# Kernel tuning notes

Hardware: AMD Instinct MI355X
Metric: run time of the kernel (lower is better)

## Reference

```python
import jax, jax.numpy as jnp
import numpy as np

D_MODEL = 512
TEMP = 30.0  # softmax temperature used by TransformerTrack-style RelationUnit
EPS = 1e-5
NORM_SCALE = float(np.sqrt(1.0 / (D_MODEL * 4 * 4)))


def _instance_l2norm(x):
    # x: [n, hw, b, d]; InstanceL2Norm over (dim, h, w) per (image, batch) sample
    n, hw, b, d = x.shape
    ss = jnp.sum(x * x, axis=(1, 3), keepdims=True)  # [n,1,b,1]
    return x * (NORM_SCALE * jnp.sqrt((d * hw) / (ss + EPS)))


def _cnorm(r, i):
    # joint L2 normalization of a complex vector along last axis
    s = jnp.sqrt(jnp.sum(r * r + i * i, axis=-1, keepdims=True) + 1e-12)
    return r / s, i / s


def _rel_self_attn(xr, xi, er, ei, WK):
    # xr/xi: [n, L, b, d]; er/ei: [n, L, L, b, dk] relative (helix) embeddings
    qr, qi = _cnorm(xr @ WK, xi @ WK)           # [n,L,b,dk]
    # real part of complex conjugate inner product <q, k>
    scores = (jnp.einsum('nqbk,nlbk->nbql', qr, qr)
              + jnp.einsum('nqbk,nlbk->nbql', qi, qi)
              + jnp.einsum('nqbk,nqlbk->nbql', qr, er)
              + jnp.einsum('nqbk,nqlbk->nbql', qi, ei))
    A = jax.nn.softmax(scores * TEMP, axis=-1)  # [n,b,q,l]
    out_r = jnp.einsum('nbql,nlbd->nqbd', A, xr)
    out_i = jnp.einsum('nbql,nlbd->nqbd', A, xi)
    return out_r, out_i


def _cross_attn(qr_in, qi_in, kr_in, ki_in, vr, vi, WK):
    # q: [Lq,b,d]; k,v: [Lk,b,d]
    qr, qi = _cnorm(qr_in @ WK, qi_in @ WK)
    kr, ki = _cnorm(kr_in @ WK, ki_in @ WK)
    scores = jnp.einsum('qbk,lbk->bql', qr, kr) + jnp.einsum('qbk,lbk->bql', qi, ki)
    A = jax.nn.softmax(scores * TEMP, axis=-1)
    out_r = jnp.einsum('bql,lbd->qbd', A, vr)
    out_i = jnp.einsum('bql,lbd->qbd', A, vi)
    return out_r, out_i


def _forward(src_real, src_imag, tgt_real, tgt_imag,
             src_emb_real, src_emb_imag, tgt_emb_real, tgt_emb_imag,
             pos_real, pos_imag, WK_rel, WK_cross):
    n, b, d, h, w = src_real.shape
    hw = h * w

    def tok(x):  # [n,b,d,h,w] -> [n,hw,b,d]
        return x.reshape(n, b, d, hw).transpose(0, 3, 1, 2)

    def emb(x):  # [n,b,dk,hw,hw] -> [n,hw,hw,b,dk]
        return x.transpose(0, 3, 4, 1, 2)

    sr, si = tok(src_real), tok(src_imag)
    tr, ti = tok(tgt_real), tok(tgt_imag)
    esr, esi = emb(src_emb_real), emb(src_emb_imag)
    etr, eti = emb(tgt_emb_real), emb(tgt_emb_imag)

    # ---- encoder (num_layers = 1) ----
    s2r, s2i = _rel_self_attn(sr, si, esr, esi, WK_rel)
    mem_r = _instance_l2norm(sr + s2r).reshape(n * hw, b, d)
    mem_i = _instance_l2norm(si + s2i).reshape(n * hw, b, d)

    # pos: [n,b,h,w] -> [n*hw, b, d] (broadcast over dim as in .repeat(1,1,dim))
    pr = jnp.broadcast_to(pos_real.reshape(n, b, hw).transpose(0, 2, 1).reshape(n * hw, b, 1), (n * hw, b, d))
    pi = jnp.broadcast_to(pos_imag.reshape(n, b, hw).transpose(0, 2, 1).reshape(n * hw, b, 1), (n * hw, b, d))

    def IN3(x):
        return _instance_l2norm(x.reshape(n, hw, b, d)).reshape(n * hw, b, d)

    # ---- decoder (num_layers = 1) ----
    t2r, t2i = _rel_self_attn(tr, ti, etr, eti, WK_rel)
    xr = _instance_l2norm(tr + t2r).reshape(n * hw, b, d)
    xi = _instance_l2norm(ti + t2i).reshape(n * hw, b, d)

    mask_r, mask_i = _cross_attn(xr, xi, mem_r, mem_i, pr, pi, WK_cross)
    y2r = IN3(xr * mask_r)
    y2i = IN3(xi * mask_i)

    t3r, t3i = _cross_attn(xr, xi, mem_r, mem_i, mem_r * pr, mem_i * pi, WK_cross)
    y4r = IN3(xr + t3r)
    y4i = IN3(xi + t3i)

    out_r = IN3(y2r + y4r)
    out_i = IN3(y2i + y4i)

    feat_r = out_r.reshape(n, h, w, b, d).transpose(0, 3, 4, 1, 2).reshape(n * b, d, h, w)
    feat_i = out_i.reshape(n, h, w, b, d).transpose(0, 3, 4, 1, 2).reshape(n * b, d, h, w)
    return out_r, out_i, feat_r, feat_i


def setup_inputs() -> dict:
    key = jax.random.key(0)
    ks = jax.random.split(key, 12)
    n, b, d, h, dk = 2, 2, 512, 16, 64
    hw = h * h
    inp = {
        'src_real': jax.random.normal(ks[0], (n, b, d, h, h), jnp.float32),
        'src_imag': jax.random.normal(ks[1], (n, b, d, h, h), jnp.float32),
        'tgt_real': jax.random.normal(ks[2], (n, b, d, h, h), jnp.float32),
        'tgt_imag': jax.random.normal(ks[3], (n, b, d, h, h), jnp.float32),
        'src_emb_real': jax.random.normal(ks[4], (n, b, dk, hw, hw), jnp.float32),
        'src_emb_imag': jax.random.normal(ks[5], (n, b, dk, hw, hw), jnp.float32),
        'tgt_emb_real': jax.random.normal(ks[6], (n, b, dk, hw, hw), jnp.float32),
        'tgt_emb_imag': jax.random.normal(ks[7], (n, b, dk, hw, hw), jnp.float32),
        'pos_real': jax.random.uniform(ks[8], (n, b, h, h), jnp.float32),
        'pos_imag': jax.random.uniform(ks[9], (n, b, h, h), jnp.float32),
        'WK_rel': jax.random.normal(ks[10], (d, dk), jnp.float32) * 0.02,
        'WK_cross': jax.random.normal(ks[11], (d, 128), jnp.float32) * 0.02,
    }
    return inp


def reference(src_real, src_imag, tgt_real, tgt_imag,
              src_emb_real, src_emb_imag, tgt_emb_real, tgt_emb_imag,
              pos_real, pos_imag, WK_rel, WK_cross):
    return _forward(src_real, src_imag, tgt_real, tgt_imag,
                    src_emb_real, src_emb_imag, tgt_emb_real, tgt_emb_imag,
                    pos_real, pos_imag, WK_rel, WK_cross)
```

## Files before the change

### kernel.cpp

```cpp
#include <hip/hip_runtime.h>
#include <cstdint>
#include <cstddef>

#define N_ 2
#define B_ 2
#define D_ 512
#define HW_ 256
#define DK_ 64
#define DKC_ 128
#define G_ 4
#define NBLK_ 32

constexpr size_t OFF_TSR = 0;
constexpr size_t OFF_TSI = 524288;
constexpr size_t OFF_TTR = 1048576;
constexpr size_t OFF_TTI = 1572864;
constexpr size_t OFF_QSR = 2097152;
constexpr size_t OFF_QSI = OFF_QSR + 65536;
constexpr size_t OFF_QTR = OFF_QSI + 65536;
constexpr size_t OFF_QTI = OFF_QTR + 65536;
constexpr size_t OFF_AS  = OFF_QTI + 65536;
constexpr size_t OFF_AT  = OFF_AS + 262144;
constexpr size_t OFF_YSR = OFF_AT + 262144;
constexpr size_t OFF_YSI = OFF_YSR + 524288;
constexpr size_t OFF_YTR = OFF_YSI + 524288;
constexpr size_t OFF_YTI = OFF_YTR + 524288;
constexpr size_t OFF_QCR = OFF_YTI + 524288;
constexpr size_t OFF_QCI = OFF_QCR + 131072;
constexpr size_t OFF_KCR = OFF_QCI + 131072;
constexpr size_t OFF_KCI = OFF_KCR + 131072;
constexpr size_t OFF_AC  = OFF_KCI + 131072;
constexpr size_t OFF_T3R = OFF_AC + 524288;
constexpr size_t OFF_T3I = OFF_T3R + 524288;
constexpr size_t OFF_MR  = OFF_T3I + 524288;
constexpr size_t OFF_MI  = OFF_MR + 1024;
constexpr size_t OFF_P1  = OFF_MI + 1024;
constexpr size_t OFF_P2  = OFF_P1 + 512;
constexpr size_t OFF_P3  = OFF_P2 + 512;
constexpr size_t OFF_S1  = OFF_P3 + 256;
constexpr size_t OFF_S2  = OFF_S1 + 16;
constexpr size_t OFF_SZ  = OFF_S2 + 16;

template<int NT>
__device__ __forceinline__ float blk_sum(float v, float* sh) {
  int tid = threadIdx.x;
  sh[tid] = v; __syncthreads();
  #pragma unroll
  for (int s = NT/2; s > 0; s >>= 1) { if (tid < s) sh[tid] += sh[tid+s]; __syncthreads(); }
  float r = sh[0]; __syncthreads(); return r;
}
template<int NT>
__device__ __forceinline__ float blk_max(float v, float* sh) {
  int tid = threadIdx.x;
  sh[tid] = v; __syncthreads();
  #pragma unroll
  for (int s = NT/2; s > 0; s >>= 1) { if (tid < s) sh[tid] = fmaxf(sh[tid], sh[tid+s]); __syncthreads(); }
  float r = sh[0]; __syncthreads(); return r;
}

__global__ void k_transpose(const float* sR, const float* sI, const float* tR, const float* tI, float* ws) {
  int which = blockIdx.y;
  const float* in = (which==0)? sR : (which==1)? sI : (which==2)? tR : tI;
  float* out = ws + ((which==0)? OFF_TSR : (which==1)? OFF_TSI : (which==2)? OFF_TTR : OFF_TTI);
  int bx = blockIdx.x;
  int pt = bx & 3, dt = (bx>>2)&7, nb = bx>>5;
  int ni = nb>>1, bi = nb&1;
  __shared__ float tile[64][65];
  int tid = threadIdx.x;
  int p0 = pt*64, d0 = dt*64;
  #pragma unroll
  for (int it=0; it<16; ++it) {
    int i = it*256 + tid; int row = i>>6, col = i&63;
    tile[row][col] = in[(size_t)(nb*D_ + d0+row)*HW_ + p0+col];
  }
  __syncthreads();
  #pragma unroll
  for (int it=0; it<16; ++it) {
    int i = it*256 + tid; int row = i>>6, col = i&63;
    out[(size_t)((ni*HW_ + p0+row)*B_ + bi)*D_ + d0+col] = tile[col][row];
  }
}

__global__ void k_qrel(float* ws, const float* WK) {
  int idx = blockIdx.x;
  int which = idx >> 10; int t = idx & 1023;
  int r = t >> 1, bi = t & 1;
  const float* Tr = ws + (which ? OFF_TTR : OFF_TSR);
  const float* Ti = ws + (which ? OFF_TTI : OFF_TSI);
  float* Qr = ws + (which ? OFF_QTR : OFF_QSR);
  float* Qi = ws + (which ? OFF_QTI : OFF_QSI);
  int tid = threadIdx.x;
  int kk = tid & 63, isIm = tid >> 6;
  const float* x = (isIm ? Ti : Tr) + (size_t)(r*B_ + bi)*D_;
  const float4* x4 = (const float4*)x;
  float acc = 0.f;
  #pragma unroll 8
  for (int d4 = 0; d4 < 128; ++d4) {
    float4 xv = x4[d4]; int d = d4*4;
    acc += xv.x*WK[(d+0)*DK_+kk] + xv.y*WK[(d+1)*DK_+kk] + xv.z*WK[(d+2)*DK_+kk] + xv.w*WK[(d+3)*DK_+kk];
  }
  __shared__ float sh[128];
  float ss = blk_sum<128>(acc*acc, sh);
  float q = acc / sqrtf(ss + 1e-12f);
  (isIm ? Qi : Qr)[(size_t)(r*B_ + bi)*DK_ + kk] = q;
}

__global__ void __launch_bounds__(128) k_gram(float* ws) {
  int bx = blockIdx.x;
  int lt = bx & 3, qt = (bx>>2)&7, nb = (bx>>5)&3, which = bx>>7;
  int ni = nb>>1, bi = nb&1;
  const float* Qr = ws + (which ? OFF_QTR : OFF_QSR);
  const float* Qi = ws + (which ? OFF_QTI : OFF_QSI);
  float* A = ws + (which ? OFF_AT : OFF_AS) + (size_t)nb*65536;
  __shared__ float Qrs[32][33], Qis[32][33], Krs[32][68], Kis[32][68];
  int tid = threadIdx.x, ty = tid>>4, tx = tid&15;
  int ty4 = ty*4, tx4 = tx*4;
  float acc[4][4] = {};
  for (int c = 0; c < 2; ++c) {
    #pragma unroll
    for (int it = 0; it < 8; ++it) {
      int i = it*128 + tid; int row = i>>5, col = i&31;
      size_t qa = (size_t)((ni*HW_ + qt*32+row)*B_ + bi)*DK_ + c*32 + col;
      Qrs[row][col] = Qr[qa];
      Qis[row][col] = Qi[qa];
    }
    #pragma unroll
    for (int it = 0; it < 16; ++it) {
      int i = it*128 + tid; int kk = i&31, col = i>>5;
      size_t ka = (size_t)((ni*HW_ + lt*64+col)*B_ + bi)*DK_ + c*32 + kk;
      Krs[kk][col] = Qr[ka];
      Kis[kk][col] = Qi[ka];
    }
    __syncthreads();
    #pragma unroll
    for (int kk = 0; kk < 32; ++kk) {
      float4 kr = *(const float4*)&Krs[kk][tx4];
      float4 ki = *(const float4*)&Kis[kk][tx4];
      #pragma unroll
      for (int i = 0; i < 4; ++i) {
        float qr = Qrs[ty4+i][kk], qi = Qis[ty4+i][kk];
        acc[i][0] += qr*kr.x + qi*ki.x;
        acc[i][1] += qr*kr.y + qi*ki.y;
        acc[i][2] += qr*kr.z + qi*ki.z;
        acc[i][3] += qr*kr.w + qi*ki.w;
      }
    }
    __syncthreads();
  }
  #pragma unroll
  for (int i = 0; i < 4; ++i)
    #pragma unroll
    for (int j = 0; j < 4; ++j)
      A[(size_t)(qt*32+ty4+i)*256 + lt*64+tx4+j] = acc[i][j];
}

__global__ void __launch_bounds__(256) k_selfattn(float* ws, const float* esr, const float* esi,
                                                  const float* etr, const float* eti) {
  int idx = blockIdx.x;
  int iq = idx & 255, nb = (idx>>8)&3, which = idx>>10;
  int ni = nb>>1, bi = nb&1;
  const float* Qr = ws + (which ? OFF_QTR : OFF_QSR);
  const float* Qi = ws + (which ? OFF_QTI : OFF_QSI);
  const float* er = which ? etr : esr;
  const float* ei = which ? eti : esi;
  float* Arow = ws + (which ? OFF_AT : OFF_AS) + (size_t)nb*65536 + (size_t)iq*256;
  int tid = threadIdx.x, w = tid>>6, lane = tid&63;
  size_t qbase = (size_t)((ni*HW_ + iq)*B_ + bi)*DK_ + w*16;
  int kl = lane & 15;
  float qv = ((lane & 16) ? Qi : Qr)[qbase + kl];
  int l0 = lane*4;
  float a0=0.f, a1=0.f, a2=0.f, a3=0.f;
  size_t eb = (size_t)nb*4194304 + (size_t)(w*16)*65536 + (size_t)iq*256 + l0;
  #pragma unroll 4
  for (int kk = 0; kk < 16; ++kk) {
    float4 e4r = *(const float4*)&er[eb + (size_t)kk*65536];
    float4 e4i = *(const float4*)&ei[eb + (size_t)kk*65536];
    float fr = __shfl(qv, kk);
    float fi = __shfl(qv, 16+kk);
    a0 += fr*e4r.x + fi*e4i.x;
    a1 += fr*e4r.y + fi*e4i.y;
    a2 += fr*e4r.z + fi*e4i.z;
    a3 += fr*e4r.w + fi*e4i.w;
  }
  __shared__ float part[4][256];
  __shared__ float sh[256];
  *(float4*)&part[w][l0] = make_float4(a0,a1,a2,a3);
  __syncthreads();
  float s = (part[0][tid]+part[1][tid]+part[2][tid]+part[3][tid] + Arow[tid]) * 30.f;
  float m = blk_max<256>(s, sh);
  float e = __expf(s - m);
  float sum = blk_sum<256>(e, sh);
  Arow[tid] = e / sum;
}

__global__ void __launch_bounds__(128) k_selfapply(float* ws) {
  int bx = blockIdx.x;
  int dt = bx & 7, qt = (bx>>3)&7, nb = (bx>>6)&3, which = bx>>8;
  int ni = nb>>1, bi = nb&1;
  const float* A  = ws + (which ? OFF_AT : OFF_AS) + (size_t)nb*65536;
  const float* Xr = ws + (which ? OFF_TTR : OFF_TSR);
  const float* Xi = ws + (which ? OFF_TTI : OFF_TSI);
  float* Yr = ws + (which ? OFF_YTR : OFF_YSR);
  float* Yi = ws + (which ? OFF_YTI : OFF_YSI);
  __shared__ float As[32][33], Xrs[32][68], Xis[32][68];
  int tid = threadIdx.x, ty = tid>>4, tx = tid&15;
  int ty4 = ty*4, tx4 = tx*4;
  float ar[4][4] = {}, ai[4][4] = {};
  for (int c = 0; c < 8; ++c) {
    #pragma unroll
    for (int it = 0; it < 8; ++it) {
      int i = it*128 + tid; int row = i>>5, col = i&31;
      As[row][col] = A[(size_t)(qt*32+row)*256 + c*32+col];
    }
    #pragma unroll
    for (int it = 0; it < 16; ++it) {
      int i = it*128 + tid; int row = i>>6, col = i&63;
      size_t xb = (size_t)((ni*HW_ + c*32+row)*B_ + bi)*D_ + dt*64+col;
      Xrs[row][col] = Xr[xb]; Xis[row][col] = Xi[xb];
    }
    __syncthreads();
    #pragma unroll
    for (int kk = 0; kk < 32; ++kk) {
      float4 vr = *(const float4*)&Xrs[kk][tx4];
      float4 vi = *(const float4*)&Xis[kk][tx4];
      #pragma unroll
      for (int i = 0; i < 4; ++i) {
        float a = As[ty4+i][kk];
        ar[i][0] += a*vr.x; ar[i][1] += a*vr.y; ar[i][2] += a*vr.z; ar[i][3] += a*vr.w;
        ai[i][0] += a*vi.x; ai[i][1] += a*vi.y; ai[i][2] += a*vi.z; ai[i][3] += a*vi.w;
      }
    }
    __syncthreads();
  }
  #pragma unroll
  for (int i = 0; i < 4; ++i) {
    size_t o = (size_t)((ni*HW_ + qt*32 + ty4+i)*B_ + bi)*D_ + dt*64 + tx4;
    #pragma unroll
    for (int j = 0; j < 4; ++j) { Yr[o+j] = Xr[o+j] + ar[i][j]; Yi[o+j] = Xi[o+j] + ai[i][j]; }
  }
}

__global__ void k_reduce4(float* ws) {
  int qy = blockIdx.y;
  const float* a = ws + ((qy==0)? OFF_YSR : (qy==1)? OFF_YSI : (qy==2)? OFF_YTR : OFF_YTI);
  int g = blockIdx.x / NBLK_, blk = blockIdx.x % NBLK_;
  int ni = g>>1, bi = g&1;
  int tid = threadIdx.x;
  float acc = 0.f;
  for (int p = blk; p < HW_; p += NBLK_) {
    const float* row = a + (size_t)((ni*HW_ + p)*B_ + bi)*D_;
    for (int d = tid; d < D_; d += 256) { float v = row[d]; acc += v*v; }
  }
  __shared__ float sh[256];
  float s = blk_sum<256>(acc, sh);
  if (!tid) ws[OFF_P1 + (size_t)(qy*G_ + g)*NBLK_ + blk] = s;
}

__global__ void k_finalize(const float* part, float* scales, int nq) {
  int t = threadIdx.x;
  if (t < nq) {
    float ss = 0.f;
    for (int j = 0; j < NBLK_; ++j) ss += part[t*NBLK_ + j];
    scales[t] = 4.f * rsqrtf(ss + 1e-5f);
  }
}

__global__ void k_applyscale(float* ws, const float* scales) {
  int qy = blockIdx.y;
  float* a = ws + ((qy==0)? OFF_YSR : (qy==1)? OFF_YSI : (qy==2)? OFF_YTR : OFF_YTI);
  int idx4 = blockIdx.x*256 + threadIdx.x;
  int elem = idx4*4;
  int bi = (elem / D_) & 1;
  int r = elem >> 10;
  int ni = r >> 8;
  float s = scales[qy*G_ + ni*2 + bi];
  float4 v = ((float4*)a)[idx4];
  v.x *= s; v.y *= s; v.z *= s; v.w *= s;
  ((float4*)a)[idx4] = v;
}

__global__ void k_crossproj(float* ws, const float* W) {
  int idx = blockIdx.x;
  int isK = idx >> 10; int t = idx & 1023;
  int r = t >> 1, bi = t & 1;
  const float* inR = ws + (isK ? OFF_YSR : OFF_YTR);
  const float* inI = ws + (isK ? OFF_YSI : OFF_YTI);
  float* oR = ws + (isK ? OFF_KCR : OFF_QCR);
  float* oI = ws + (isK ? OFF_KCI : OFF_QCI);
  int tid = threadIdx.x;
  const float4* xr4 = (const float4*)(inR + (size_t)(r*B_ + bi)*D_);
  const float4* xi4 = (const float4*)(inI + (size_t)(r*B_ + bi)*D_);
  float aR = 0.f, aI = 0.f;
  #pragma unroll 8
  for (int d4 = 0; d4 < 128; ++d4) {
    float4 rv = xr4[d4], iv = xi4[d4]; int d = d4*4;
    float w0 = W[(d+0)*DKC_ + tid], w1 = W[(d+1)*DKC_ + tid], w2 = W[(d+2)*DKC_ + tid], w3 = W[(d+3)*DKC_ + tid];
    aR += rv.x*w0 + rv.y*w1 + rv.z*w2 + rv.w*w3;
    aI += iv.x*w0 + iv.y*w1 + iv.z*w2 + iv.w*w3;
  }
  __shared__ float sh[128];
  float ss = blk_sum<128>(aR*aR + aI*aI, sh);
  float inv = 1.f / sqrtf(ss + 1e-12f);
  oR[(size_t)(r*B_ + bi)*DKC_ + tid] = aR * inv;
  oI[(size_t)(r*B_ + bi)*DKC_ + tid] = aI * inv;
}

__global__ void __launch_bounds__(128) k_crossscore(float* ws) {
  int bx = blockIdx.x;
  int lt = bx & 7, qt = (bx>>3)&15, bi = bx>>7;
  const float* Qr = ws + OFF_QCR; const float* Qi = ws + OFF_QCI;
  const float* Kr = ws + OFF_KCR; const float* Ki = ws + OFF_KCI;
  float* S = ws + OFF_AC + (size_t)bi*262144;
  __shared__ float Qrs[32][33], Qis[32][33], Krs[32][68], Kis[32][68];
  int tid = threadIdx.x, ty = tid>>4, tx = tid&15;
  int ty4 = ty*4, tx4 = tx*4;
  float acc[4][4] = {};
  for (int c = 0; c < 4; ++c) {
    #pragma unroll
    for (int it = 0; it < 8; ++it) {
      int i = it*128 + tid; int row = i>>5, col = i&31;
      Qrs[row][col] = Qr[(size_t)((qt*32+row)*B_ + bi)*DKC_ + c*32 + col];
      Qis[row][col] = Qi[(size_t)((qt*32+row)*B_ + bi)*DKC_ + c*32 + col];
    }
    #pragma unroll
    for (int it = 0; it < 16; ++it) {
      int i = it*128 + tid; int kk = i&31, col = i>>5;
      Krs[kk][col] = Kr[(size_t)((lt*64+col)*B_ + bi)*DKC_ + c*32 + kk];
      Kis[kk][col] = Ki[(size_t)((lt*64+col)*B_ + bi)*DKC_ + c*32 + kk];
    }
    __syncthreads();
    #pragma unroll
    for (int kk = 0; kk < 32; ++kk) {
      float4 kr = *(const float4*)&Krs[kk][tx4];
      float4 ki = *(const float4*)&Kis[kk][tx4];
      #pragma unroll
      for (int i = 0; i < 4; ++i) {
        float qr = Qrs[ty4+i][kk], qi = Qis[ty4+i][kk];
        acc[i][0] += qr*kr.x + qi*ki.x;
        acc[i][1] += qr*kr.y + qi*ki.y;
        acc[i][2] += qr*kr.z + qi*ki.z;
        acc[i][3] += qr*kr.w + qi*ki.w;
      }
    }
    __syncthreads();
  }
  #pragma unroll
  for (int i = 0; i < 4; ++i)
    #pragma unroll
    for (int j = 0; j < 4; ++j)
      S[(size_t)(qt*32+ty4+i)*512 + lt*64+tx4+j] = acc[i][j];
}

__global__ void k_softmaxrow(float* ws, const float* posr, const float* posi) {
  int bx = blockIdx.x;
  int bi = bx >> 9, iq = bx & 511;
  float* row = ws + OFF_AC + (size_t)bi*262144 + (size_t)iq*512;
  int tid = threadIdx.x;
  float s0 = row[tid]*30.f, s1 = row[tid+256]*30.f;
  __shared__ float sh[256];
  float m = blk_max<256>(fmaxf(s0, s1), sh);
  float e0 = __expf(s0 - m), e1 = __expf(s1 - m);
  float sum = blk_sum<256>(e0 + e1, sh);
  float inv = 1.f / sum;
  float a0 = e0*inv, a1 = e1*inv;
  row[tid] = a0; row[tid+256] = a1;
  float pr0 = posr[bi*HW_ + tid],        pr1 = posr[(B_+bi)*HW_ + tid];
  float pi0 = posi[bi*HW_ + tid],        pi1 = posi[(B_+bi)*HW_ + tid];
  float mr = blk_sum<256>(a0*pr0 + a1*pr1, sh);
  float mi = blk_sum<256>(a0*pi0 + a1*pi1, sh);
  if (!tid) { ws[OFF_MR + bi*512 + iq] = mr; ws[OFF_MI + bi*512 + iq] = mi; }
}

__global__ void __launch_bounds__(128) k_crossapply(float* ws, const float* posr, const float* posi) {
  int bx = blockIdx.x;
  int dt = bx & 7, qt = (bx>>3)&15, bi = (bx>>7)&1, kc = bx>>8;
  const float* A  = ws + OFF_AC + (size_t)bi*262144;
  const float* Mr = ws + OFF_YSR; const float* Mi = ws + OFF_YSI;
  float* Pr = ws + (kc ? OFF_TSR : OFF_T3R);
  float* Pi = ws + (kc ? OFF_TSI : OFF_T3I);
  __shared__ float As[32][33], Vrs[32][68], Vis[32][68];
  int tid = threadIdx.x, ty = tid>>4, tx = tid&15;
  int ty4 = ty*4, tx4 = tx*4;
  float ar[4][4] = {}, ai[4][4] = {};
  for (int c = 0; c < 8; ++c) {
    int kb = kc*256 + c*32;
    #pragma unroll
    for (int it = 0; it < 8; ++it) {
      int i = it*128 + tid; int row = i>>5, col = i&31;
      As[row][col] = A[(size_t)(qt*32+row)*512 + kb+col];
    }
    #pragma unroll
    for (int it = 0; it < 16; ++it) {
      int i = it*128 + tid; int row = i>>6, col = i&63;
      int l = kb + row; int nil = l>>8, pl = l&255;
      float pvr = posr[(nil*B_ + bi)*HW_ + pl];
      float pvi = posi[(nil*B_ + bi)*HW_ + pl];
      size_t vb = (size_t)(l*B_ + bi)*D_ + dt*64+col;
      Vrs[row][col] = Mr[vb] * pvr;
      Vis[row][col] = Mi[vb] * pvi;
    }
    __syncthreads();
    #pragma unroll
    for (int kk = 0; kk < 32; ++kk) {
      float4 vr = *(const float4*)&Vrs[kk][tx4];
      float4 vi = *(const float4*)&Vis[kk][tx4];
      #pragma unroll
      for (int i = 0; i < 4; ++i) {
        float a = As[ty4+i][kk];
        ar[i][0] += a*vr.x; ar[i][1] += a*vr.y; ar[i][2] += a*vr.z; ar[i][3] += a*vr.w;
        ai[i][0] += a*vi.x; ai[i][1] += a*vi.y; ai[i][2] += a*vi.z; ai[i][3] += a*vi.w;
      }
    }
    __syncthreads();
  }
  #pragma unroll
  for (int i = 0; i < 4; ++i) {
    size_t o = (size_t)((qt*32+ty4+i)*B_ + bi)*D_ + dt*64 + tx4;
    #pragma unroll
    for (int j = 0; j < 4; ++j) { Pr[o+j] = ar[i][j]; Pi[o+j] = ai[i][j]; }
  }
}

__global__ void k_reducey24(float* ws) {
  int qy = blockIdx.y;
  int g = blockIdx.x / NBLK_, blk = blockIdx.x % NBLK_;
  int ni = g>>1, bi = g&1;
  const float* X   = ws + ((qy==0 || qy==2) ? OFF_YTR : OFF_YTI);
  const float* T3a = ws + ((qy==2) ? OFF_T3R : OFF_T3I);
  const float* T3b = ws + ((qy==2) ? OFF_TSR : OFF_TSI);
  const float* M   = ws + ((qy==0) ? OFF_MR : OFF_MI);
  int tid = threadIdx.x;
  float acc = 0.f;
  for (int p = blk; p < HW_; p += NBLK_) {
    int l = ni*HW_ + p;
    size_t rb = (size_t)(l*B_ + bi)*D_;
    if (qy < 2) {
      float m = M[bi*512 + l];
      for (int d = tid; d < D_; d += 256) { float v = X[rb+d]*m; acc += v*v; }
    } else {
      for (int d = tid; d < D_; d += 256) { float v = X[rb+d] + T3a[rb+d] + T3b[rb+d]; acc += v*v; }
    }
  }
  __shared__ float sh[256];
  float s = blk_sum<256>(acc, sh);
  if (!tid) ws[OFF_P2 + (size_t)(qy*G_ + g)*NBLK_ + blk] = s;
}

__global__ void k_combine(float* ws, const float* scales2) {
  int y = blockIdx.y;
  int g = blockIdx.x / NBLK_, blk = blockIdx.x % NBLK_;
  int ni = g>>1, bi = g&1;
  const float* X   = ws + (y ? OFF_YTI : OFF_YTR);
  float* T3a       = ws + (y ? OFF_T3I : OFF_T3R);
  const float* T3b = ws + (y ? OFF_TSI : OFF_TSR);
  const float* M   = ws + (y ? OFF_MI : OFF_MR);
  float a2 = scales2[y*G_ + g], a4 = scales2[(2+y)*G_ + g];
  int tid = threadIdx.x;
  float acc = 0.f;
  for (int p = blk; p < HW_; p += NBLK_) {
    int l = ni*HW_ + p;
    float m = M[bi*512 + l];
    size_t rb = (size_t)(l*B_ + bi)*D_;
    for (int d = tid; d < D_; d += 256) {
      float x = X[rb+d];
      float z = a2*(x*m) + a4*(x + T3a[rb+d] + T3b[rb+d]);
      T3a[rb+d] = z;
      acc += z*z;
    }
  }
  __shared__ float sh[256];
  float s = blk_sum<256>(acc, sh);
  if (!tid) ws[OFF_P3 + (size_t)(y*G_ + g)*NBLK_ + blk] = s;
}

__global__ void k_final(float* ws, const float* scalesZ, float* out) {
  int y = blockIdx.y;
  int bx = blockIdx.x;
  int pt = bx & 3, dt = (bx>>2)&7, nb = bx>>5;
  int ni = nb>>1, bi = nb&1;
  const float* Z = ws + (y ? OFF_T3I : OFF_T3R);
  float s = scalesZ[y*G_ + nb];
  float* o1 = out + (size_t)y*524288;
  float* o2 = out + (size_t)(2+y)*524288;
  __shared__ float tile[64][65];
  int tid = threadIdx.x;
  int p0 = pt*64, d0 = dt*64;
  #pragma unroll
  for (int it = 0; it < 16; ++it) {
    int i = it*256 + tid; int row = i>>6, col = i&63;
    size_t idx = (size_t)((ni*HW_ + p0+row)*B_ + bi)*D_ + d0+col;
    float v = Z[idx] * s;
    o1[idx] = v;
    tile[row][col] = v;
  }
  __syncthreads();
  #pragma unroll
  for (int it = 0; it < 16; ++it) {
    int i = it*256 + tid; int row = i>>6, col = i&63;
    o2[(size_t)(nb*D_ + d0+row)*HW_ + p0+col] = tile[col][row];
  }
}

extern "C" void kernel_launch(void* const* d_in, const int* in_sizes, int n_in,
                              void* d_out, int out_size, void* d_ws, size_t ws_size,
                              hipStream_t stream) {
  const float* srcR = (const float*)d_in[0];
  const float* srcI = (const float*)d_in[1];
  const float* tgtR = (const float*)d_in[2];
  const float* tgtI = (const float*)d_in[3];
  const float* esr  = (const float*)d_in[4];
  const float* esi  = (const float*)d_in[5];
  const float* etr  = (const float*)d_in[6];
  const float* eti  = (const float*)d_in[7];
  const float* posR = (const float*)d_in[8];
  const float* posI = (const float*)d_in[9];
  const float* WKrel   = (const float*)d_in[10];
  const float* WKcross = (const float*)d_in[11];
  float* ws  = (float*)d_ws;
  float* out = (float*)d_out;

  k_transpose <<<dim3(128,4), 256, 0, stream>>>(srcR, srcI, tgtR, tgtI, ws);
  k_qrel      <<<2048, 128, 0, stream>>>(ws, WKrel);
  k_gram      <<<256, 128, 0, stream>>>(ws);
  k_selfattn  <<<2048, 256, 0, stream>>>(ws, esr, esi, etr, eti);
  k_selfapply <<<512, 128, 0, stream>>>(ws);
  k_reduce4   <<<dim3(G_*NBLK_,4), 256, 0, stream>>>(ws);
  k_finalize  <<<1, 64, 0, stream>>>(ws + OFF_P1, ws + OFF_S1, 16);
  k_applyscale<<<dim3(512,4), 256, 0, stream>>>(ws, ws + OFF_S1);
  k_crossproj <<<2048, 128, 0, stream>>>(ws, WKcross);
  k_crossscore<<<256, 128, 0, stream>>>(ws);
  k_softmaxrow<<<1024, 256, 0, stream>>>(ws, posR, posI);
  k_crossapply<<<512, 128, 0, stream>>>(ws, posR, posI);
  k_reducey24 <<<dim3(G_*NBLK_,4), 256, 0, stream>>>(ws);
  k_finalize  <<<1, 64, 0, stream>>>(ws + OFF_P2, ws + OFF_S2, 16);
  k_combine   <<<dim3(G_*NBLK_,2), 256, 0, stream>>>(ws, ws + OFF_S2);
  k_finalize  <<<1, 64, 0, stream>>>(ws + OFF_P3, ws + OFF_SZ, 8);
  k_final     <<<dim3(128,2), 256, 0, stream>>>(ws, ws + OFF_SZ, out);
}
```

Measured before the change: 275.0 us.

## Tile projection kernels over 8 rows and batch embedding loads in selfattn

The q-projection and cross-projection kernels now stage 8 token rows of real and imaginary input in shared memory and have each thread compute 2 or 4 output columns for both parts. Each weight row read is reused across real and imaginary parts, the block-wide reduction becomes a 32-lane shuffle reduction, and the block count drops eightfold. The self-attention kernel loads q into shared memory and issues all 16 embedding float4 loads per component up front to expose memory-level parallelism. The cost is higher register pressure, which the launch bound of 256 threads with 2 blocks tries to keep in check.

Measured after the change: 290.2 us. +5.6%, slower.

```diff
diff --git a/kernel.cpp b/kernel.cpp
--- a/kernel.cpp
+++ b/kernel.cpp
@@ -57,6 +57,11 @@
   for (int s = NT/2; s > 0; s >>= 1) { if (tid < s) sh[tid] = fmaxf(sh[tid], sh[tid+s]); __syncthreads(); }
   float r = sh[0]; __syncthreads(); return r;
 }
+__device__ __forceinline__ float wave_sum32(float v) {
+  #pragma unroll
+  for (int o = 16; o; o >>= 1) v += __shfl_xor(v, o, 64);
+  return v;
+}
 
 __global__ void k_transpose(const float* sR, const float* sI, const float* tR, const float* tI, float* ws) {
   int which = blockIdx.y;
@@ -81,28 +86,39 @@
   }
 }
 
-__global__ void k_qrel(float* ws, const float* WK) {
-  int idx = blockIdx.x;
-  int which = idx >> 10; int t = idx & 1023;
-  int r = t >> 1, bi = t & 1;
+__global__ void __launch_bounds__(256) k_qrel(float* ws, const float* WK) {
+  int bx = blockIdx.x;
+  int rg = bx & 127, which = bx >> 7;
   const float* Tr = ws + (which ? OFF_TTR : OFF_TSR);
   const float* Ti = ws + (which ? OFF_TTI : OFF_TSI);
   float* Qr = ws + (which ? OFF_QTR : OFF_QSR);
   float* Qi = ws + (which ? OFF_QTI : OFF_QSI);
-  int tid = threadIdx.x;
-  int kk = tid & 63, isIm = tid >> 6;
-  const float* x = (isIm ? Ti : Tr) + (size_t)(r*B_ + bi)*D_;
-  const float4* x4 = (const float4*)x;
-  float acc = 0.f;
-  #pragma unroll 8
-  for (int d4 = 0; d4 < 128; ++d4) {
-    float4 xv = x4[d4]; int d = d4*4;
-    acc += xv.x*WK[(d+0)*DK_+kk] + xv.y*WK[(d+1)*DK_+kk] + xv.z*WK[(d+2)*DK_+kk] + xv.w*WK[(d+3)*DK_+kk];
-  }
-  __shared__ float sh[128];
-  float ss = blk_sum<128>(acc*acc, sh);
-  float q = acc / sqrtf(ss + 1e-12f);
-  (isIm ? Qi : Qr)[(size_t)(r*B_ + bi)*DK_ + kk] = q;
+  int R0 = rg*8;
+  __shared__ float Xr[8][512], Xi[8][512];
+  int tid = threadIdx.x;
+  const float4* tr4 = (const float4*)(Tr + (size_t)R0*D_);
+  const float4* ti4 = (const float4*)(Ti + (size_t)R0*D_);
+  #pragma unroll
+  for (int it=0; it<4; ++it) {
+    int i = it*256 + tid;
+    ((float4*)&Xr[0][0])[i] = tr4[i];
+    ((float4*)&Xi[0][0])[i] = ti4[i];
+  }
+  __syncthreads();
+  int row = tid >> 5, col2 = (tid & 31)*2;
+  float a0r=0.f, a0i=0.f, a1r=0.f, a1i=0.f;
+  #pragma unroll 4
+  for (int d=0; d<512; ++d) {
+    float2 w = *(const float2*)&WK[(size_t)d*DK_ + col2];
+    float xr = Xr[row][d], xi = Xi[row][d];
+    a0r += xr*w.x; a1r += xr*w.y;
+    a0i += xi*w.x; a1i += xi*w.y;
+  }
+  float ss = wave_sum32(a0r*a0r + a1r*a1r + a0i*a0i + a1i*a1i);
+  float inv = 1.f / sqrtf(ss + 1e-12f);
+  size_t o = (size_t)(R0+row)*DK_ + col2;
+  Qr[o]   = a0r*inv; Qr[o+1] = a1r*inv;
+  Qi[o]   = a0i*inv; Qi[o+1] = a1i*inv;
 }
 
 __global__ void __launch_bounds__(128) k_gram(float* ws) {
@@ -154,8 +170,8 @@
       A[(size_t)(qt*32+ty4+i)*256 + lt*64+tx4+j] = acc[i][j];
 }
 
-__global__ void __launch_bounds__(256) k_selfattn(float* ws, const float* esr, const float* esi,
-                                                  const float* etr, const float* eti) {
+__global__ void __launch_bounds__(256, 2) k_selfattn(float* ws, const float* esr, const float* esi,
+                                                     const float* etr, const float* eti) {
   int idx = blockIdx.x;
   int iq = idx & 255, nb = (idx>>8)&3, which = idx>>10;
   int ni = nb>>1, bi = nb&1;
@@ -164,23 +180,31 @@
   const float* er = which ? etr : esr;
   const float* ei = which ? eti : esi;
   float* Arow = ws + (which ? OFF_AT : OFF_AS) + (size_t)nb*65536 + (size_t)iq*256;
+  __shared__ float qqr[64], qqi[64];
   int tid = threadIdx.x, w = tid>>6, lane = tid&63;
-  size_t qbase = (size_t)((ni*HW_ + iq)*B_ + bi)*DK_ + w*16;
-  int kl = lane & 15;
-  float qv = ((lane & 16) ? Qi : Qr)[qbase + kl];
+  int tokq = ni*HW_ + iq;
+  if (tid < 64)       qqr[tid]    = Qr[(size_t)(tokq*B_ + bi)*DK_ + tid];
+  else if (tid < 128) qqi[tid-64] = Qi[(size_t)(tokq*B_ + bi)*DK_ + (tid-64)];
+  __syncthreads();
+  float fr[16], fi[16];
+  #pragma unroll
+  for (int kk = 0; kk < 16; ++kk) { fr[kk] = qqr[w*16+kk]; fi[kk] = qqi[w*16+kk]; }
   int l0 = lane*4;
+  size_t eb = (size_t)nb*4194304 + (size_t)(w*16)*65536 + (size_t)iq*256 + l0;
+  const float4* er4 = (const float4*)&er[eb];
+  const float4* ei4 = (const float4*)&ei[eb];
+  float4 R[16], I[16];
+  #pragma unroll
+  for (int t = 0; t < 16; ++t) R[t] = er4[(size_t)t*16384];
+  #pragma unroll
+  for (int t = 0; t < 16; ++t) I[t] = ei4[(size_t)t*16384];
   float a0=0.f, a1=0.f, a2=0.f, a3=0.f;
-  size_t eb = (size_t)nb*4194304 + (size_t)(w*16)*65536 + (size_t)iq*256 + l0;
-  #pragma unroll 4
-  for (int kk = 0; kk < 16; ++kk) {
-    float4 e4r = *(const float4*)&er[eb + (size_t)kk*65536];
-    float4 e4i = *(const float4*)&ei[eb + (size_t)kk*65536];
-    float fr = __shfl(qv, kk);
-    float fi = __shfl(qv, 16+kk);
-    a0 += fr*e4r.x + fi*e4i.x;
-    a1 += fr*e4r.y + fi*e4i.y;
-    a2 += fr*e4r.z + fi*e4i.z;
-    a3 += fr*e4r.w + fi*e4i.w;
+  #pragma unroll
+  for (int t = 0; t < 16; ++t) {
+    a0 += fr[t]*R[t].x + fi[t]*I[t].x;
+    a1 += fr[t]*R[t].y + fi[t]*I[t].y;
+    a2 += fr[t]*R[t].z + fi[t]*I[t].z;
+    a3 += fr[t]*R[t].w + fi[t]*I[t].w;
   }
   __shared__ float part[4][256];
   __shared__ float sh[256];
@@ -279,30 +303,41 @@
   ((float4*)a)[idx4] = v;
 }
 
-__global__ void k_crossproj(float* ws, const float* W) {
-  int idx = blockIdx.x;
-  int isK = idx >> 10; int t = idx & 1023;
-  int r = t >> 1, bi = t & 1;
+__global__ void __launch_bounds__(256) k_crossproj(float* ws, const float* W) {
+  int bx = blockIdx.x;
+  int rg = bx & 127, isK = bx >> 7;
   const float* inR = ws + (isK ? OFF_YSR : OFF_YTR);
   const float* inI = ws + (isK ? OFF_YSI : OFF_YTI);
   float* oR = ws + (isK ? OFF_KCR : OFF_QCR);
   float* oI = ws + (isK ? OFF_KCI : OFF_QCI);
-  int tid = threadIdx.x;
-  const float4* xr4 = (const float4*)(inR + (size_t)(r*B_ + bi)*D_);
-  const float4* xi4 = (const float4*)(inI + (size_t)(r*B_ + bi)*D_);
-  float aR = 0.f, aI = 0.f;
-  #pragma unroll 8
-  for (int d4 = 0; d4 < 128; ++d4) {
-    float4 rv = xr4[d4], iv = xi4[d4]; int d = d4*4;
-    float w0 = W[(d+0)*DKC_ + tid], w1 = W[(d+1)*DKC_ + tid], w2 = W[(d+2)*DKC_ + tid], w3 = W[(d+3)*DKC_ + tid];
-    aR += rv.x*w0 + rv.y*w1 + rv.z*w2 + rv.w*w3;
-    aI += iv.x*w0 + iv.y*w1 + iv.z*w2 + iv.w*w3;
-  }
-  __shared__ float sh[128];
-  float ss = blk_sum<128>(aR*aR + aI*aI, sh);
+  int R0 = rg*8;
+  __shared__ float Xr[8][512], Xi[8][512];
+  int tid = threadIdx.x;
+  const float4* xr4 = (const float4*)(inR + (size_t)R0*D_);
+  const float4* xi4 = (const float4*)(inI + (size_t)R0*D_);
+  #pragma unroll
+  for (int it=0; it<4; ++it) {
+    int i = it*256 + tid;
+    ((float4*)&Xr[0][0])[i] = xr4[i];
+    ((float4*)&Xi[0][0])[i] = xi4[i];
+  }
+  __syncthreads();
+  int row = tid >> 5, col4 = (tid & 31)*4;
+  float ar[4]={}, ai[4]={};
+  #pragma unroll 4
+  for (int d=0; d<512; ++d) {
+    float4 w = *(const float4*)&W[(size_t)d*DKC_ + col4];
+    float xr = Xr[row][d], xi = Xi[row][d];
+    ar[0] += xr*w.x; ar[1] += xr*w.y; ar[2] += xr*w.z; ar[3] += xr*w.w;
+    ai[0] += xi*w.x; ai[1] += xi*w.y; ai[2] += xi*w.z; ai[3] += xi*w.w;
+  }
+  float ps = ar[0]*ar[0]+ar[1]*ar[1]+ar[2]*ar[2]+ar[3]*ar[3]
+           + ai[0]*ai[0]+ai[1]*ai[1]+ai[2]*ai[2]+ai[3]*ai[3];
+  float ss = wave_sum32(ps);
   float inv = 1.f / sqrtf(ss + 1e-12f);
-  oR[(size_t)(r*B_ + bi)*DKC_ + tid] = aR * inv;
-  oI[(size_t)(r*B_ + bi)*DKC_ + tid] = aI * inv;
+  size_t o = (size_t)(R0+row)*DKC_ + col4;
+  oR[o]   = ar[0]*inv; oR[o+1] = ar[1]*inv; oR[o+2] = ar[2]*inv; oR[o+3] = ar[3]*inv;
+  oI[o]   = ai[0]*inv; oI[o+1] = ai[1]*inv; oI[o+2] = ai[2]*inv; oI[o+3] = ai[3]*inv;
 }
 
 __global__ void __launch_bounds__(128) k_crossscore(float* ws) {
@@ -520,14 +555,14 @@
   float* out = (float*)d_out;
 
   k_transpose <<<dim3(128,4), 256, 0, stream>>>(srcR, srcI, tgtR, tgtI, ws);
-  k_qrel      <<<2048, 128, 0, stream>>>(ws, WKrel);
+  k_qrel      <<<256, 256, 0, stream>>>(ws, WKrel);
   k_gram      <<<256, 128, 0, stream>>>(ws);
   k_selfattn  <<<2048, 256, 0, stream>>>(ws, esr, esi, etr, eti);
   k_selfapply <<<512, 128, 0, stream>>>(ws);
   k_reduce4   <<<dim3(G_*NBLK_,4), 256, 0, stream>>>(ws);
   k_finalize  <<<1, 64, 0, stream>>>(ws + OFF_P1, ws + OFF_S1, 16);
   k_applyscale<<<dim3(512,4), 256, 0, stream>>>(ws, ws + OFF_S1);
-  k_crossproj <<<2048, 128, 0, stream>>>(ws, WKcross);
+  k_crossproj <<<256, 256, 0, stream>>>(ws, WKcross);
   k_crossscore<<<256, 128, 0, stream>>>(ws);
   k_softmaxrow<<<1024, 256, 0, stream>>>(ws, posR, posI);
   k_crossapply<<<512, 128, 0, stream>>>(ws, posR, posI);
```
